# Performance work log

Hardware: AMD Instinct MI355X
Metric: run time of the kernel (lower is better)

## Reference

```python
import jax, jax.numpy as jnp
import numpy as np
from jax import lax

N = 25600      # total nodes = G * T
E = 204800     # edges (before self loops)
IN_CH = 6
HID = 64
HEADS = 4
G = 512        # graphs per batch
T = 50         # sequence length (node_time in [0, T))
OUT = 30       # prediction_horizon * 3
NEG_SLOPE = 0.2
BN_EPS = 1e-5


def _gat(x, src, dst, W, a_src, a_dst, b, heads, outc):
    # PyG GATConv (concat=True): h = x W reshaped to (N, H, C)
    n = x.shape[0]
    h = (x @ W).reshape(n, heads, outc)
    # edge scores: leaky_relu(a_src . h_src + a_dst . h_dst), softmax over incoming edges of dst
    e = jax.nn.leaky_relu((h * a_src).sum(-1)[src] + (h * a_dst).sum(-1)[dst], NEG_SLOPE)  # (E, H)
    m = jax.ops.segment_max(e, dst, num_segments=n)
    ex = jnp.exp(e - m[dst])
    denom = jax.ops.segment_sum(ex, dst, num_segments=n)
    alpha = ex / denom[dst]
    out = jax.ops.segment_sum(alpha[:, :, None] * h[src], dst, num_segments=n)  # (N, H, C)
    return out.reshape(n, heads * outc) + b


def _bn_eval(x, g, b):
    # BatchNorm in eval with running_mean=0, running_var=1
    return g * (x * (1.0 / np.float32(np.sqrt(1.0 + BN_EPS)))) + b


def setup_inputs() -> dict:
    ks = jax.random.split(jax.random.key(0), 16)
    s = 0.1
    d = {}
    d["x"] = jax.random.normal(ks[0], (N, IN_CH), jnp.float32)
    d["edge_index"] = jax.random.randint(ks[1], (2, E), 0, N)
    idx = jnp.arange(N)
    d["batch"] = idx // T       # each graph has exactly T nodes
    d["node_time"] = idx % T
    d["W1"] = jax.random.normal(ks[2], (IN_CH, HEADS * HID), jnp.float32) * s
    d["att_src1"] = jax.random.normal(ks[3], (HEADS, HID), jnp.float32) * s
    d["att_dst1"] = jax.random.normal(ks[4], (HEADS, HID), jnp.float32) * s
    d["b1"] = jnp.zeros((HEADS * HID,), jnp.float32)
    d["g1"] = jnp.ones((HEADS * HID,), jnp.float32)
    d["be1"] = jnp.zeros((HEADS * HID,), jnp.float32)
    d["W2"] = jax.random.normal(ks[5], (HEADS * HID, HID), jnp.float32) * s
    d["att_src2"] = jax.random.normal(ks[6], (1, HID), jnp.float32) * s
    d["att_dst2"] = jax.random.normal(ks[7], (1, HID), jnp.float32) * s
    d["b2"] = jnp.zeros((HID,), jnp.float32)
    d["g2"] = jnp.ones((HID,), jnp.float32)
    d["be2"] = jnp.zeros((HID,), jnp.float32)
    d["Wih"] = jax.random.normal(ks[8], (4 * HID, HID), jnp.float32) * s
    d["Whh"] = jax.random.normal(ks[9], (4 * HID, HID), jnp.float32) * s
    d["bih"] = jnp.zeros((4 * HID,), jnp.float32)
    d["bhh"] = jnp.zeros((4 * HID,), jnp.float32)
    d["Wfc"] = jax.random.normal(ks[10], (HID, OUT), jnp.float32) * s
    d["bfc"] = jnp.zeros((OUT,), jnp.float32)
    return d


def reference(x, edge_index, batch, node_time, W1, att_src1, att_dst1, b1, g1, be1,
              W2, att_src2, att_dst2, b2, g2, be2, Wih, Whh, bih, bhh, Wfc, bfc):
    loops = jnp.arange(N)
    src = jnp.concatenate([edge_index[0], loops])  # GATConv adds self loops
    dst = jnp.concatenate([edge_index[1], loops])
    h = jax.nn.elu(_bn_eval(_gat(x, src, dst, W1, att_src1, att_dst1, b1, HEADS, HID), g1, be1))
    h = jax.nn.elu(_bn_eval(_gat(h, src, dst, W2, att_src2, att_dst2, b2, 1, HID), g2, be2))
    # vectorized replacement of the per-node python scatter loop
    x_seq = jnp.zeros((G, T, HID), h.dtype).at[batch, node_time].set(h)

    def step(carry, xt):
        hh, cc = carry
        gates = xt @ Wih.T + bih + hh @ Whh.T + bhh
        i, f, gg, o = jnp.split(gates, 4, axis=-1)
        cc = jax.nn.sigmoid(f) * cc + jax.nn.sigmoid(i) * jnp.tanh(gg)
        hh = jax.nn.sigmoid(o) * jnp.tanh(cc)
        return (hh, cc), None

    init = (jnp.zeros((G, HID), h.dtype), jnp.zeros((G, HID), h.dtype))
    (hn, _), _ = lax.scan(step, init, x_seq.transpose(1, 0, 2))  # scan over time
    return hn @ Wfc + bfc  # (G, 30)
```

## Files before the change

kernel.cpp:

```cpp
#include <hip/hip_runtime.h>

#define N_NODES 25600
#define N_EDGES 204800
#define EE (N_EDGES + N_NODES)
#define IN_CH 6
#define HID 64
#define HEADS 4
#define G_GRAPHS 512
#define T_STEPS 50
#define OUT_DIM 30
#define NEG_SLOPE 0.2f
#define BN_INV 0.9999950000374997f

__device__ __forceinline__ float lrelu_(float x){ return x > 0.f ? x : NEG_SLOPE * x; }
__device__ __forceinline__ float elu_(float x){ return x > 0.f ? x : __expf(x) - 1.f; }
__device__ __forceinline__ float sigmoid_(float x){
    return __builtin_amdgcn_rcpf(1.f + __expf(-x));
}
__device__ __forceinline__ float tanh_(float x){
    return 1.f - 2.f * __builtin_amdgcn_rcpf(1.f + __expf(2.f * x));
}

__global__ void count_k(const int* __restrict__ ei, int* __restrict__ counts){
    int e = blockIdx.x * 256 + threadIdx.x;
    if (e >= EE) return;
    int dst = (e < N_EDGES) ? ei[N_EDGES + e] : (e - N_EDGES);
    atomicAdd(&counts[dst], 1);
}

__global__ void scan_k(const int* __restrict__ counts, int* __restrict__ row_ptr,
                       int* __restrict__ cursor){
    __shared__ int part[1024];
    int t = threadIdx.x;
    const int CH = N_NODES / 1024;
    int base = t * CH;
    int s = 0;
    for (int i = 0; i < CH; i++) s += counts[base + i];
    part[t] = s;
    __syncthreads();
    for (int off = 1; off < 1024; off <<= 1){
        int v = (t >= off) ? part[t - off] : 0;
        __syncthreads();
        part[t] += v;
        __syncthreads();
    }
    int run = (t > 0) ? part[t - 1] : 0;
    for (int i = 0; i < CH; i++){
        int cv = counts[base + i];
        row_ptr[base + i] = run;
        cursor[base + i]  = run;
        run += cv;
    }
    if (t == 1023) row_ptr[N_NODES] = run;
}

__global__ void scatter_k(const int* __restrict__ ei, int* __restrict__ cursor,
                          int* __restrict__ ssrc){
    int e = blockIdx.x * 256 + threadIdx.x;
    if (e >= EE) return;
    int src, dst;
    if (e < N_EDGES){ src = ei[e]; dst = ei[N_EDGES + e]; }
    else            { src = dst = e - N_EDGES; }
    int pos = atomicAdd(&cursor[dst], 1);
    ssrc[pos] = src;
}

__global__ void wa_k(const float* __restrict__ W1, const float* __restrict__ asw,
                     const float* __restrict__ adw, float* __restrict__ waS,
                     float* __restrict__ waD){
    int t = threadIdx.x;
    if (t >= 48) return;
    int k = t >> 3, h = (t >> 1) & 3, which = t & 1;
    const float* a = which ? adw : asw;
    float s = 0.f;
    #pragma unroll
    for (int c = 0; c < 64; c++) s += W1[k * 256 + h * 64 + c] * a[h * 64 + c];
    (which ? waD : waS)[k * 4 + h] = s;
}

__global__ void ns_k(const float* __restrict__ x, const float* __restrict__ waS,
                     const float* __restrict__ waD, float* __restrict__ as1,
                     float* __restrict__ ad1){
    int n = blockIdx.x * 256 + threadIdx.x;
    float xv[IN_CH];
    #pragma unroll
    for (int k = 0; k < IN_CH; k++) xv[k] = x[n * IN_CH + k];
    float sv[4] = {0.f, 0.f, 0.f, 0.f}, dv[4] = {0.f, 0.f, 0.f, 0.f};
    #pragma unroll
    for (int k = 0; k < IN_CH; k++){
        #pragma unroll
        for (int h = 0; h < 4; h++){
            sv[h] += xv[k] * waS[k * 4 + h];
            dv[h] += xv[k] * waD[k * 4 + h];
        }
    }
    *(float4*)&as1[n * 4] = make_float4(sv[0], sv[1], sv[2], sv[3]);
    *(float4*)&ad1[n * 4] = make_float4(dv[0], dv[1], dv[2], dv[3]);
}

__global__ void gat1_aggx(const float* __restrict__ x, const float* __restrict__ as1,
                          const float* __restrict__ ad1, const int* __restrict__ row_ptr,
                          const int* __restrict__ ssrc, const float* __restrict__ W1,
                          const float* __restrict__ b1, const float* __restrict__ g1,
                          const float* __restrict__ be1, float* __restrict__ h1_act){
    __shared__ float w1s[IN_CH * 256];
    int tid = threadIdx.x;
    for (int i = tid; i < IN_CH * 256; i += 256) w1s[i] = W1[i];
    __syncthreads();
    int wv = tid >> 6, lane = tid & 63;
    int n = blockIdx.x * 4 + wv;
    int s0 = row_ptr[n], s1 = row_ptr[n + 1];
    float4 adn = *(const float4*)&ad1[n * 4];
    float xs0[IN_CH] = {}, xs1[IN_CH] = {}, xs2[IN_CH] = {}, xs3[IN_CH] = {};
    float d0 = 0.f, d1 = 0.f, d2 = 0.f, d3 = 0.f;
    for (int j = s0; j < s1; j++){
        int s = ssrc[j];
        float4 as = *(const float4*)&as1[s * 4];
        float e0 = __expf(lrelu_(as.x + adn.x));
        float e1 = __expf(lrelu_(as.y + adn.y));
        float e2 = __expf(lrelu_(as.z + adn.z));
        float e3 = __expf(lrelu_(as.w + adn.w));
        d0 += e0; d1 += e1; d2 += e2; d3 += e3;
        const float2* xp = (const float2*)(x + (size_t)s * IN_CH);
        float2 xa = xp[0], xb = xp[1], xc = xp[2];
        float xv[IN_CH] = {xa.x, xa.y, xb.x, xb.y, xc.x, xc.y};
        #pragma unroll
        for (int k = 0; k < IN_CH; k++){
            xs0[k] += e0 * xv[k];
            xs1[k] += e1 * xv[k];
            xs2[k] += e2 * xv[k];
            xs3[k] += e3 * xv[k];
        }
    }
    float r0 = 1.f / d0, r1 = 1.f / d1, r2 = 1.f / d2, r3 = 1.f / d3;
    #pragma unroll
    for (int h = 0; h < 4; h++){
        const float* xsh = (h == 0) ? xs0 : (h == 1) ? xs1 : (h == 2) ? xs2 : xs3;
        float rh = (h == 0) ? r0 : (h == 1) ? r1 : (h == 2) ? r2 : r3;
        int col = h * 64 + lane;
        float acc = 0.f;
        #pragma unroll
        for (int k = 0; k < IN_CH; k++) acc += xsh[k] * w1s[k * 256 + col];
        float v = acc * rh + b1[col];
        v = g1[col] * (v * BN_INV) + be1[col];
        h1_act[(size_t)n * 256 + col] = elu_(v);
    }
}

#define TM 64
#define KT 32
#define APAD 4
__global__ __launch_bounds__(256) void gat2_tr(const float* __restrict__ h1_act,
                        const float* __restrict__ W2,
                        const float* __restrict__ asw, const float* __restrict__ adw,
                        float* __restrict__ h2_pre, float* __restrict__ as2,
                        float* __restrict__ ad2){
    __shared__ float As[TM][KT + APAD];
    __shared__ float Bs[KT][64];
    int tx = threadIdx.x;
    int rg = tx >> 4;
    int cg = tx & 15;
    int r0 = rg * 4, c0 = cg * 4;
    int rowBase = blockIdx.x * TM;
    float acc[4][4] = {};
    for (int k0 = 0; k0 < 256; k0 += KT){
        #pragma unroll
        for (int it = 0; it < 2; it++){
            int i = tx + it * 256;
            int row = i >> 3;
            int c4  = (i & 7) * 4;
            *(float4*)&As[row][c4] =
                *(const float4*)(h1_act + (size_t)(rowBase + row) * 256 + k0 + c4);
        }
        #pragma unroll
        for (int it = 0; it < 2; it++){
            int i = tx + it * 256;
            int row = i >> 4;
            int c4  = (i & 15) * 4;
            *(float4*)&Bs[row][c4] = *(const float4*)(W2 + (size_t)(k0 + row) * 64 + c4);
        }
        __syncthreads();
        #pragma unroll
        for (int kq = 0; kq < KT; kq += 4){
            float4 b0 = *(float4*)&Bs[kq + 0][c0];
            float4 b1v = *(float4*)&Bs[kq + 1][c0];
            float4 b2v = *(float4*)&Bs[kq + 2][c0];
            float4 b3 = *(float4*)&Bs[kq + 3][c0];
            #pragma unroll
            for (int i = 0; i < 4; i++){
                float4 a = *(float4*)&As[r0 + i][kq];
                acc[i][0] += a.x * b0.x + a.y * b1v.x + a.z * b2v.x + a.w * b3.x;
                acc[i][1] += a.x * b0.y + a.y * b1v.y + a.z * b2v.y + a.w * b3.y;
                acc[i][2] += a.x * b0.z + a.y * b1v.z + a.z * b2v.z + a.w * b3.z;
                acc[i][3] += a.x * b0.w + a.y * b1v.w + a.z * b2v.w + a.w * b3.w;
            }
        }
        __syncthreads();
    }
    float aw0 = asw[c0], aw1 = asw[c0+1], aw2 = asw[c0+2], aw3 = asw[c0+3];
    float dw0 = adw[c0], dw1 = adw[c0+1], dw2 = adw[c0+2], dw3 = adw[c0+3];
    #pragma unroll
    for (int i = 0; i < 4; i++){
        int row = rowBase + r0 + i;
        *(float4*)(h2_pre + (size_t)row * 64 + c0) =
            make_float4(acc[i][0], acc[i][1], acc[i][2], acc[i][3]);
        float sA = acc[i][0]*aw0 + acc[i][1]*aw1 + acc[i][2]*aw2 + acc[i][3]*aw3;
        float sD = acc[i][0]*dw0 + acc[i][1]*dw1 + acc[i][2]*dw2 + acc[i][3]*dw3;
        #pragma unroll
        for (int off = 8; off; off >>= 1){
            sA += __shfl_xor(sA, off);
            sD += __shfl_xor(sD, off);
        }
        if (cg == 0){ as2[row] = sA; ad2[row] = sD; }
    }
}

__global__ void gat2_agg(const float* __restrict__ h2_pre, const float* __restrict__ as2,
                         const float* __restrict__ ad2, const int* __restrict__ row_ptr,
                         const int* __restrict__ ssrc,
                         const float* __restrict__ b2, const float* __restrict__ g2,
                         const float* __restrict__ be2,
                         const int* __restrict__ batch, const int* __restrict__ ntime,
                         float* __restrict__ xseq){
    int wv = threadIdx.x >> 6, lane = threadIdx.x & 63;
    int n = blockIdx.x * 4 + wv;
    int s0 = row_ptr[n], s1 = row_ptr[n + 1];
    float adn = ad2[n];
    float denom = 0.f, acc = 0.f;
    for (int j = s0; j < s1; j++){
        int s = ssrc[j];
        float e = __expf(lrelu_(as2[s] + adn));
        denom += e;
        acc += e * h2_pre[(size_t)s * 64 + lane];
    }
    float v = acc / denom + b2[lane];
    v = g2[lane] * (v * BN_INV) + be2[lane];
    v = elu_(v);
    int pos = batch[n] * T_STEPS + ntime[n];
    xseq[(size_t)pos * 64 + lane] = v;
}

__global__ __launch_bounds__(256) void gx_k(const float* __restrict__ xseq,
        const float* __restrict__ Wih, const float* __restrict__ bih,
        const float* __restrict__ bhh, float* __restrict__ gx){
    __shared__ float As[64][68];
    __shared__ float Bs[64][128];
    int tx = threadIdx.x;
    int rowBase = blockIdx.x * 64;
    int colBase = blockIdx.y * 128;
    #pragma unroll
    for (int it = 0; it < 4; it++){
        int i = tx + it * 256;
        int r = i >> 4;
        int c4 = (i & 15) * 4;
        *(float4*)&As[r][c4] = *(const float4*)(xseq + (size_t)(rowBase + r) * 64 + c4);
    }
    #pragma unroll
    for (int it = 0; it < 8; it++){
        int i = tx + it * 256;
        int jj = i & 127;
        int k4 = (i >> 7) * 4;
        float4 wv = *(const float4*)(Wih + (size_t)(colBase + jj) * 64 + k4);
        Bs[k4 + 0][jj] = wv.x;
        Bs[k4 + 1][jj] = wv.y;
        Bs[k4 + 2][jj] = wv.z;
        Bs[k4 + 3][jj] = wv.w;
    }
    __syncthreads();
    int rg = tx >> 5;
    int cg = tx & 31;
    int r0 = rg * 8, c0 = cg * 4;
    float acc[8][4] = {};
    #pragma unroll
    for (int kq = 0; kq < 64; kq += 4){
        float4 b0 = *(float4*)&Bs[kq + 0][c0];
        float4 b1 = *(float4*)&Bs[kq + 1][c0];
        float4 b2 = *(float4*)&Bs[kq + 2][c0];
        float4 b3 = *(float4*)&Bs[kq + 3][c0];
        #pragma unroll
        for (int i = 0; i < 8; i++){
            float4 a = *(float4*)&As[r0 + i][kq];
            acc[i][0] += a.x * b0.x + a.y * b1.x + a.z * b2.x + a.w * b3.x;
            acc[i][1] += a.x * b0.y + a.y * b1.y + a.z * b2.y + a.w * b3.y;
            acc[i][2] += a.x * b0.z + a.y * b1.z + a.z * b2.z + a.w * b3.z;
            acc[i][3] += a.x * b0.w + a.y * b1.w + a.z * b2.w + a.w * b3.w;
        }
    }
    int col = colBase + c0;
    float4 bb = make_float4(bih[col] + bhh[col], bih[col+1] + bhh[col+1],
                            bih[col+2] + bhh[col+2], bih[col+3] + bhh[col+3]);
    #pragma unroll
    for (int i = 0; i < 8; i++){
        int row = rowBase + r0 + i;
        *(float4*)(gx + (size_t)row * 256 + col) =
            make_float4(acc[i][0] + bb.x, acc[i][1] + bb.y,
                        acc[i][2] + bb.z, acc[i][3] + bb.w);
    }
}

__global__ __launch_bounds__(256, 2) void lstm_k(const float* __restrict__ gx,
        const float* __restrict__ Whh,
        const float* __restrict__ Wfc, const float* __restrict__ bfc,
        float* __restrict__ out){
    int g = blockIdx.x;
    int j = threadIdx.x;
    int wv = j >> 6, lane = j & 63;
    __shared__ float gates[2][256];
    __shared__ float hb[4][2][64];
    float4 whh[16];
    const float4* Hr = (const float4*)(Whh + j * 64);
    #pragma unroll
    for (int k = 0; k < 16; k++) whh[k] = Hr[k];
    float c = 0.f;
    hb[wv][0][lane] = 0.f;
    const float* gxg = gx + (size_t)g * T_STEPS * 256;
    float gxv = gxg[j];
    float hn = 0.f;
    for (int t = 0; t < T_STEPS; t++){
        float gx_next = (t + 1 < T_STEPS) ? gxg[(t + 1) * 256 + j] : 0.f;
        int buf = t & 1;
        const float4* hp = (const float4*)hb[wv][buf];
        float a0 = gxv, a1 = 0.f, a2 = 0.f, a3 = 0.f;
        #pragma unroll
        for (int k = 0; k < 16; k++){
            float4 hv = hp[k];
            float4 wvv = whh[k];
            a0 += wvv.x * hv.x;
            a1 += wvv.y * hv.y;
            a2 += wvv.z * hv.z;
            a3 += wvv.w * hv.w;
        }
        gates[buf][j] = (a0 + a1) + (a2 + a3);
        __syncthreads();
        float iv = gates[buf][lane];
        float fv = gates[buf][64 + lane];
        float gv = gates[buf][128 + lane];
        float ov = gates[buf][192 + lane];
        c = sigmoid_(fv) * c + sigmoid_(iv) * tanh_(gv);
        hn = sigmoid_(ov) * tanh_(c);
        hb[wv][buf ^ 1][lane] = hn;
        gxv = gx_next;
    }
    if (wv == 0) gates[0][lane] = hn;
    __syncthreads();
    if (j < OUT_DIM){
        float acc = bfc[j];
        #pragma unroll
        for (int k = 0; k < 64; k++) acc += gates[0][k] * Wfc[k * OUT_DIM + j];
        out[g * OUT_DIM + j] = acc;
    }
}

extern "C" void kernel_launch(void* const* d_in, const int* in_sizes, int n_in,
                              void* d_out, int out_size, void* d_ws, size_t ws_size,
                              hipStream_t stream){
    const float* x    = (const float*)d_in[0];
    const int*   ei   = (const int*)  d_in[1];
    const int*   batch= (const int*)  d_in[2];
    const int*   ntime= (const int*)  d_in[3];
    const float* W1   = (const float*)d_in[4];
    const float* as1w = (const float*)d_in[5];
    const float* ad1w = (const float*)d_in[6];
    const float* b1   = (const float*)d_in[7];
    const float* g1   = (const float*)d_in[8];
    const float* be1  = (const float*)d_in[9];
    const float* W2   = (const float*)d_in[10];
    const float* as2w = (const float*)d_in[11];
    const float* ad2w = (const float*)d_in[12];
    const float* b2   = (const float*)d_in[13];
    const float* g2   = (const float*)d_in[14];
    const float* be2  = (const float*)d_in[15];
    const float* Wih  = (const float*)d_in[16];
    const float* Whh  = (const float*)d_in[17];
    const float* bih  = (const float*)d_in[18];
    const float* bhh  = (const float*)d_in[19];
    const float* Wfc  = (const float*)d_in[20];
    const float* bfc  = (const float*)d_in[21];
    float* out = (float*)d_out;

    char* w = (char*)d_ws;
    auto alloc = [&](size_t bytes)->char*{
        char* p = w;
        w += (bytes + 255) & ~size_t(255);
        return p;
    };
    float* h1_act = (float*)alloc((size_t)N_NODES * 256 * 4);
    float* gx     = (float*)alloc((size_t)N_NODES * 256 * 4);
    float* h2_pre = (float*)alloc((size_t)N_NODES * 64 * 4);
    float* xseq   = (float*)alloc((size_t)G_GRAPHS * T_STEPS * 64 * 4);
    float* as1    = (float*)alloc((size_t)N_NODES * 4 * 4);
    float* ad1    = (float*)alloc((size_t)N_NODES * 4 * 4);
    float* as2    = (float*)alloc((size_t)N_NODES * 4);
    float* ad2    = (float*)alloc((size_t)N_NODES * 4);
    float* waS    = (float*)alloc(IN_CH * 4 * 4);
    float* waD    = (float*)alloc(IN_CH * 4 * 4);
    int* counts   = (int*)alloc((size_t)N_NODES * 4);
    int* row_ptr  = (int*)alloc((size_t)(N_NODES + 1) * 4);
    int* cursor   = (int*)alloc((size_t)N_NODES * 4);
    int* ssrc     = (int*)alloc((size_t)EE * 4);

    hipMemsetAsync(counts, 0, (size_t)N_NODES * 4, stream);
    count_k  <<<(EE + 255) / 256, 256, 0, stream>>>(ei, counts);
    scan_k   <<<1, 1024, 0, stream>>>(counts, row_ptr, cursor);
    scatter_k<<<(EE + 255) / 256, 256, 0, stream>>>(ei, cursor, ssrc);
    wa_k     <<<1, 64, 0, stream>>>(W1, as1w, ad1w, waS, waD);
    ns_k     <<<N_NODES / 256, 256, 0, stream>>>(x, waS, waD, as1, ad1);
    gat1_aggx<<<N_NODES / 4, 256, 0, stream>>>(x, as1, ad1, row_ptr, ssrc, W1, b1, g1, be1, h1_act);
    gat2_tr  <<<N_NODES / TM, 256, 0, stream>>>(h1_act, W2, as2w, ad2w, h2_pre, as2, ad2);
    gat2_agg <<<N_NODES / 4, 256, 0, stream>>>(h2_pre, as2, ad2, row_ptr, ssrc, b2, g2, be2, batch, ntime, xseq);
    gx_k     <<<dim3(N_NODES / 64, 2), 256, 0, stream>>>(xseq, Wih, bih, bhh, gx);
    lstm_k   <<<G_GRAPHS, 256, 0, stream>>>(gx, Whh, Wfc, bfc, out);
}
```

Measured before the change: 306.1 us.

## Fuse GAT2 aggregation with LSTM input projection and fold wa_k into ns_k

Merges the layer-2 GAT aggregation and the Wih input-gate GEMM into one kernel. Each block aggregates 16 nodes into shared memory, then each thread holds one Wih row in registers and writes gate pre-activations straight to gx at the scattered sequence position, so the xseq buffer round trip and one launch go away. The edge loop is unrolled by four for more memory-level parallelism. The tiny wa_k precompute is folded into ns_k, which recomputes it per block. In exchange, every block reloads its Wih row and uses 64 registers for it, which may cut occupancy.

```diff
diff --git a/kernel.cpp b/kernel.cpp
--- a/kernel.cpp
+++ b/kernel.cpp
@@ -65,23 +65,21 @@
     ssrc[pos] = src;
 }
 
-__global__ void wa_k(const float* __restrict__ W1, const float* __restrict__ asw,
-                     const float* __restrict__ adw, float* __restrict__ waS,
-                     float* __restrict__ waD){
+__global__ void ns_k(const float* __restrict__ x, const float* __restrict__ W1,
+                     const float* __restrict__ asw, const float* __restrict__ adw,
+                     float* __restrict__ as1, float* __restrict__ ad1){
+    __shared__ float waS[IN_CH * 4], waD[IN_CH * 4];
     int t = threadIdx.x;
-    if (t >= 48) return;
-    int k = t >> 3, h = (t >> 1) & 3, which = t & 1;
-    const float* a = which ? adw : asw;
-    float s = 0.f;
-    #pragma unroll
-    for (int c = 0; c < 64; c++) s += W1[k * 256 + h * 64 + c] * a[h * 64 + c];
-    (which ? waD : waS)[k * 4 + h] = s;
-}
-
-__global__ void ns_k(const float* __restrict__ x, const float* __restrict__ waS,
-                     const float* __restrict__ waD, float* __restrict__ as1,
-                     float* __restrict__ ad1){
-    int n = blockIdx.x * 256 + threadIdx.x;
+    if (t < 48){
+        int k = t >> 3, h = (t >> 1) & 3, which = t & 1;
+        const float* a = which ? adw : asw;
+        float s = 0.f;
+        #pragma unroll
+        for (int c = 0; c < 64; c++) s += W1[k * 256 + h * 64 + c] * a[h * 64 + c];
+        (which ? waD : waS)[k * 4 + h] = s;
+    }
+    __syncthreads();
+    int n = blockIdx.x * 256 + t;
     float xv[IN_CH];
     #pragma unroll
     for (int k = 0; k < IN_CH; k++) xv[k] = x[n * IN_CH + k];
@@ -215,86 +213,68 @@
     }
 }
 
-__global__ void gat2_agg(const float* __restrict__ h2_pre, const float* __restrict__ as2,
-                         const float* __restrict__ ad2, const int* __restrict__ row_ptr,
-                         const int* __restrict__ ssrc,
-                         const float* __restrict__ b2, const float* __restrict__ g2,
-                         const float* __restrict__ be2,
-                         const int* __restrict__ batch, const int* __restrict__ ntime,
-                         float* __restrict__ xseq){
-    int wv = threadIdx.x >> 6, lane = threadIdx.x & 63;
-    int n = blockIdx.x * 4 + wv;
-    int s0 = row_ptr[n], s1 = row_ptr[n + 1];
-    float adn = ad2[n];
-    float denom = 0.f, acc = 0.f;
-    for (int j = s0; j < s1; j++){
-        int s = ssrc[j];
-        float e = __expf(lrelu_(as2[s] + adn));
-        denom += e;
-        acc += e * h2_pre[(size_t)s * 64 + lane];
-    }
-    float v = acc / denom + b2[lane];
-    v = g2[lane] * (v * BN_INV) + be2[lane];
-    v = elu_(v);
-    int pos = batch[n] * T_STEPS + ntime[n];
-    xseq[(size_t)pos * 64 + lane] = v;
-}
-
-__global__ __launch_bounds__(256) void gx_k(const float* __restrict__ xseq,
+__global__ __launch_bounds__(256, 2) void gat2_aggp(const float* __restrict__ h2_pre,
+        const float* __restrict__ as2, const float* __restrict__ ad2,
+        const int* __restrict__ row_ptr, const int* __restrict__ ssrc,
+        const float* __restrict__ b2, const float* __restrict__ g2,
+        const float* __restrict__ be2,
+        const int* __restrict__ batch, const int* __restrict__ ntime,
         const float* __restrict__ Wih, const float* __restrict__ bih,
         const float* __restrict__ bhh, float* __restrict__ gx){
-    __shared__ float As[64][68];
-    __shared__ float Bs[64][128];
-    int tx = threadIdx.x;
-    int rowBase = blockIdx.x * 64;
-    int colBase = blockIdx.y * 128;
-    #pragma unroll
-    for (int it = 0; it < 4; it++){
-        int i = tx + it * 256;
-        int r = i >> 4;
-        int c4 = (i & 15) * 4;
-        *(float4*)&As[r][c4] = *(const float4*)(xseq + (size_t)(rowBase + r) * 64 + c4);
-    }
-    #pragma unroll
-    for (int it = 0; it < 8; it++){
-        int i = tx + it * 256;
-        int jj = i & 127;
-        int k4 = (i >> 7) * 4;
-        float4 wv = *(const float4*)(Wih + (size_t)(colBase + jj) * 64 + k4);
-        Bs[k4 + 0][jj] = wv.x;
-        Bs[k4 + 1][jj] = wv.y;
-        Bs[k4 + 2][jj] = wv.z;
-        Bs[k4 + 3][jj] = wv.w;
-    }
-    __syncthreads();
-    int rg = tx >> 5;
-    int cg = tx & 31;
-    int r0 = rg * 8, c0 = cg * 4;
-    float acc[8][4] = {};
-    #pragma unroll
-    for (int kq = 0; kq < 64; kq += 4){
-        float4 b0 = *(float4*)&Bs[kq + 0][c0];
-        float4 b1 = *(float4*)&Bs[kq + 1][c0];
-        float4 b2 = *(float4*)&Bs[kq + 2][c0];
-        float4 b3 = *(float4*)&Bs[kq + 3][c0];
-        #pragma unroll
-        for (int i = 0; i < 8; i++){
-            float4 a = *(float4*)&As[r0 + i][kq];
-            acc[i][0] += a.x * b0.x + a.y * b1.x + a.z * b2.x + a.w * b3.x;
-            acc[i][1] += a.x * b0.y + a.y * b1.y + a.z * b2.y + a.w * b3.y;
-            acc[i][2] += a.x * b0.z + a.y * b1.z + a.z * b2.z + a.w * b3.z;
-            acc[i][3] += a.x * b0.w + a.y * b1.w + a.z * b2.w + a.w * b3.w;
-        }
-    }
-    int col = colBase + c0;
-    float4 bb = make_float4(bih[col] + bhh[col], bih[col+1] + bhh[col+1],
-                            bih[col+2] + bhh[col+2], bih[col+3] + bhh[col+3]);
-    #pragma unroll
-    for (int i = 0; i < 8; i++){
-        int row = rowBase + r0 + i;
-        *(float4*)(gx + (size_t)row * 256 + col) =
-            make_float4(acc[i][0] + bb.x, acc[i][1] + bb.y,
-                        acc[i][2] + bb.z, acc[i][3] + bb.w);
+    __shared__ float vsh[16][64];
+    __shared__ int posb[16];
+    int tx = threadIdx.x, wv = tx >> 6, lane = tx & 63;
+    float4 wih[16];
+    const float4* Wr = (const float4*)(Wih + tx * 64);
+    #pragma unroll
+    for (int k = 0; k < 16; k++) wih[k] = Wr[k];
+    float bsum = bih[tx] + bhh[tx];
+    int nbase = blockIdx.x * 16;
+    for (int q = 0; q < 4; q++){
+        int n = nbase + wv * 4 + q;
+        int s0 = row_ptr[n], s1 = row_ptr[n + 1];
+        float adn = ad2[n];
+        float denom = 0.f, acc = 0.f;
+        int j = s0;
+        for (; j + 4 <= s1; j += 4){
+            int sa = ssrc[j], sb = ssrc[j + 1], sc = ssrc[j + 2], sd = ssrc[j + 3];
+            float ea = __expf(lrelu_(as2[sa] + adn));
+            float eb = __expf(lrelu_(as2[sb] + adn));
+            float ec = __expf(lrelu_(as2[sc] + adn));
+            float ed = __expf(lrelu_(as2[sd] + adn));
+            float ha = h2_pre[(size_t)sa * 64 + lane];
+            float hb = h2_pre[(size_t)sb * 64 + lane];
+            float hc = h2_pre[(size_t)sc * 64 + lane];
+            float hd = h2_pre[(size_t)sd * 64 + lane];
+            denom += (ea + eb) + (ec + ed);
+            acc += ea * ha + eb * hb + ec * hc + ed * hd;
+        }
+        for (; j < s1; j++){
+            int s = ssrc[j];
+            float e = __expf(lrelu_(as2[s] + adn));
+            denom += e;
+            acc += e * h2_pre[(size_t)s * 64 + lane];
+        }
+        float v = acc / denom + b2[lane];
+        v = g2[lane] * (v * BN_INV) + be2[lane];
+        vsh[wv * 4 + q][lane] = elu_(v);
+        if (lane == 0) posb[wv * 4 + q] = batch[n] * T_STEPS + ntime[n];
+    }
+    __syncthreads();
+    #pragma unroll
+    for (int q = 0; q < 16; q++){
+        const float4* vp = (const float4*)vsh[q];
+        float a0 = 0.f, a1 = 0.f, a2 = 0.f, a3 = 0.f;
+        #pragma unroll
+        for (int k = 0; k < 16; k++){
+            float4 vv = vp[k];
+            float4 ww = wih[k];
+            a0 += ww.x * vv.x;
+            a1 += ww.y * vv.y;
+            a2 += ww.z * vv.z;
+            a3 += ww.w * vv.w;
+        }
+        gx[(size_t)posb[q] * 256 + tx] = bsum + (a0 + a1) + (a2 + a3);
     }
 }
 
@@ -387,13 +367,10 @@
     float* h1_act = (float*)alloc((size_t)N_NODES * 256 * 4);
     float* gx     = (float*)alloc((size_t)N_NODES * 256 * 4);
     float* h2_pre = (float*)alloc((size_t)N_NODES * 64 * 4);
-    float* xseq   = (float*)alloc((size_t)G_GRAPHS * T_STEPS * 64 * 4);
     float* as1    = (float*)alloc((size_t)N_NODES * 4 * 4);
     float* ad1    = (float*)alloc((size_t)N_NODES * 4 * 4);
     float* as2    = (float*)alloc((size_t)N_NODES * 4);
     float* ad2    = (float*)alloc((size_t)N_NODES * 4);
-    float* waS    = (float*)alloc(IN_CH * 4 * 4);
-    float* waD    = (float*)alloc(IN_CH * 4 * 4);
     int* counts   = (int*)alloc((size_t)N_NODES * 4);
     int* row_ptr  = (int*)alloc((size_t)(N_NODES + 1) * 4);
     int* cursor   = (int*)alloc((size_t)N_NODES * 4);
@@ -403,11 +380,10 @@
     count_k  <<<(EE + 255) / 256, 256, 0, stream>>>(ei, counts);
     scan_k   <<<1, 1024, 0, stream>>>(counts, row_ptr, cursor);
     scatter_k<<<(EE + 255) / 256, 256, 0, stream>>>(ei, cursor, ssrc);
-    wa_k     <<<1, 64, 0, stream>>>(W1, as1w, ad1w, waS, waD);
-    ns_k     <<<N_NODES / 256, 256, 0, stream>>>(x, waS, waD, as1, ad1);
+    ns_k     <<<N_NODES / 256, 256, 0, stream>>>(x, W1, as1w, ad1w, as1, ad1);
     gat1_aggx<<<N_NODES / 4, 256, 0, stream>>>(x, as1, ad1, row_ptr, ssrc, W1, b1, g1, be1, h1_act);
     gat2_tr  <<<N_NODES / TM, 256, 0, stream>>>(h1_act, W2, as2w, ad2w, h2_pre, as2, ad2);
-    gat2_agg <<<N_NODES / 4, 256, 0, stream>>>(h2_pre, as2, ad2, row_ptr, ssrc, b2, g2, be2, batch, ntime, xseq);
-    gx_k     <<<dim3(N_NODES / 64, 2), 256, 0, stream>>>(xseq, Wih, bih, bhh, gx);
+    gat2_aggp<<<N_NODES / 16, 256, 0, stream>>>(h2_pre, as2, ad2, row_ptr, ssrc, b2, g2, be2,
+                                                batch, ntime, Wih, bih, bhh, gx);
     lstm_k   <<<G_GRAPHS, 256, 0, stream>>>(gx, Whh, Wfc, bfc, out);
 }
```

Result: faster. 291.4 us (-4.8%).
